# Performance work log

Measured on AMD Instinct MI355X. Metric: run time of the kernel, lower is better.

The kernel has to match this reference:

```python
import jax, jax.numpy as jnp
import numpy as np

NUM_DEVICES = 8  # ROUTING_ROWS


def setup_inputs() -> dict:
    key = jax.random.key(0)
    k1, k2, k3 = jax.random.split(key, 3)
    T, H, E, K = 8192, 4096, 64, 2
    input_tensor = jax.random.normal(k1, (T, H), dtype=jnp.float32)
    expert_indices = jax.random.randint(k2, (T, K), 0, E, dtype=jnp.int32)
    expert_mapping = jax.random.randint(k3, (E,), 0, NUM_DEVICES, dtype=jnp.int32)
    return {
        "input_tensor": input_tensor,
        "expert_indices": expert_indices,
        "expert_mapping": expert_mapping,
    }


def reference(input_tensor, expert_indices, expert_mapping):
    # all_to_all_dispatch: replicate each token onto every device that hosts
    # one of its selected experts. Output: [D, T, H].
    # token_devices[t, k] = device hosting expert expert_indices[t, k]
    token_devices = expert_mapping[expert_indices]            # [T, K] int
    # mask[d, t] = token t is routed to device d (via any of its top-k experts)
    device_ids = jnp.arange(NUM_DEVICES, dtype=token_devices.dtype)  # [D]
    mask = jnp.any(token_devices[None, :, :] == device_ids[:, None, None], axis=-1)  # [D, T]
    dispatched = mask[:, :, None].astype(input_tensor.dtype) * input_tensor[None, :, :]  # [D, T, H]
    return dispatched
```

## Files before the change

### kernel.cpp

```cpp
#include <hip/hip_runtime.h>


#define T_TOK 8192
#define H_DIM 4096
#define NUM_DEV 8
#define TOPK 2

typedef float vfloat4 __attribute__((ext_vector_type(4)));

__global__ __launch_bounds__(256)
void a2a_copy_rows_kernel(const float* __restrict__ input,
                          const int* __restrict__ expert_indices,
                          const int* __restrict__ expert_mapping,
                          float* __restrict__ out)
{
    const unsigned bid = blockIdx.x;
    const unsigned t   = bid >> 1;
    const unsigned k   = bid & 1;

    const int e   = expert_indices[TOPK * t + k];
    const int dev = expert_mapping[e];
    if (k == 1) {
        const int e0 = expert_indices[TOPK * t];
        if (expert_mapping[e0] == dev) return;
    }

    const vfloat4* __restrict__ in_row =
        (const vfloat4*)(input + (size_t)t * H_DIM);
    vfloat4* __restrict__ out_row =
        (vfloat4*)(out + ((size_t)dev * T_TOK + (size_t)t) * H_DIM);

#pragma unroll
    for (int i = 0; i < 4; ++i) {
        out_row[threadIdx.x + i * 256] = in_row[threadIdx.x + i * 256];
    }
}

extern "C" void kernel_launch(void* const* d_in, const int* in_sizes, int n_in,
                              void* d_out, int out_size, void* d_ws, size_t ws_size,
                              hipStream_t stream) {
    const float* input          = (const float*)d_in[0];
    const int*   expert_indices = (const int*)d_in[1];
    const int*   expert_mapping = (const int*)d_in[2];
    float*       out            = (float*)d_out;

    const size_t out_bytes = (size_t)NUM_DEV * T_TOK * H_DIM * sizeof(float);
    hipMemsetAsync(out, 0, out_bytes, stream);

    const int grid = T_TOK * TOPK;
    a2a_copy_rows_kernel<<<grid, 256, 0, stream>>>(input, expert_indices,
                                                   expert_mapping, out);
}
```

Before: 1.140 ms.

## Fuse zero-fill into dispatch kernel, writing each output row exactly once

Removes the separate full-output memset and has one block per token read its row once, then write either the row or zeros to each of the 8 device slices. This avoids writing routed rows twice and drops a launch. The cost is that every block now issues 8 row writes, with a per-device branch.

Result: no change. 1.137 ms (-0.3%).

```diff
diff --git a/kernel.cpp b/kernel.cpp
--- a/kernel.cpp
+++ b/kernel.cpp
@@ -9,30 +9,42 @@
 typedef float vfloat4 __attribute__((ext_vector_type(4)));
 
 __global__ __launch_bounds__(256)
-void a2a_copy_rows_kernel(const float* __restrict__ input,
+void a2a_dispatch_rowcast(const float* __restrict__ input,
                           const int* __restrict__ expert_indices,
                           const int* __restrict__ expert_mapping,
                           float* __restrict__ out)
 {
-    const unsigned bid = blockIdx.x;
-    const unsigned t   = bid >> 1;
-    const unsigned k   = bid & 1;
+    const unsigned t = blockIdx.x;
 
-    const int e   = expert_indices[TOPK * t + k];
-    const int dev = expert_mapping[e];
-    if (k == 1) {
-        const int e0 = expert_indices[TOPK * t];
-        if (expert_mapping[e0] == dev) return;
-    }
+    const int e0 = expert_indices[TOPK * t];
+    const int e1 = expert_indices[TOPK * t + 1];
+    const unsigned mask =
+        (1u << expert_mapping[e0]) | (1u << expert_mapping[e1]);
 
     const vfloat4* __restrict__ in_row =
         (const vfloat4*)(input + (size_t)t * H_DIM);
-    vfloat4* __restrict__ out_row =
-        (vfloat4*)(out + ((size_t)dev * T_TOK + (size_t)t) * H_DIM);
+    const vfloat4 v0 = in_row[threadIdx.x];
+    const vfloat4 v1 = in_row[threadIdx.x + 256];
+    const vfloat4 v2 = in_row[threadIdx.x + 512];
+    const vfloat4 v3 = in_row[threadIdx.x + 768];
+    const vfloat4 z  = (vfloat4)(0.f);
 
+    vfloat4* out_row = (vfloat4*)(out + (size_t)t * H_DIM);
+    const size_t slice_v4 = (size_t)T_TOK * (H_DIM / 4);
 #pragma unroll
-    for (int i = 0; i < 4; ++i) {
-        out_row[threadIdx.x + i * 256] = in_row[threadIdx.x + i * 256];
+    for (int d = 0; d < NUM_DEV; ++d) {
+        if ((mask >> d) & 1u) {
+            out_row[threadIdx.x      ] = v0;
+            out_row[threadIdx.x + 256] = v1;
+            out_row[threadIdx.x + 512] = v2;
+            out_row[threadIdx.x + 768] = v3;
+        } else {
+            out_row[threadIdx.x      ] = z;
+            out_row[threadIdx.x + 256] = z;
+            out_row[threadIdx.x + 512] = z;
+            out_row[threadIdx.x + 768] = z;
+        }
+        out_row += slice_v4;
     }
 }
 
@@ -44,10 +56,6 @@
     const int*   expert_mapping = (const int*)d_in[2];
     float*       out            = (float*)d_out;
 
-    const size_t out_bytes = (size_t)NUM_DEV * T_TOK * H_DIM * sizeof(float);
-    hipMemsetAsync(out, 0, out_bytes, stream);
-
-    const int grid = T_TOK * TOPK;
-    a2a_copy_rows_kernel<<<grid, 256, 0, stream>>>(input, expert_indices,
-                                                   expert_mapping, out);
+    a2a_dispatch_rowcast<<<T_TOK, 256, 0, stream>>>(input, expert_indices,
+                                                    expert_mapping, out);
 }
```
